# Performance work log

Hardware: AMD Instinct MI355X
Metric: run time of the kernel (lower is better)

The kernel has to match this reference:

```python
import jax, jax.numpy as jnp
import numpy as np

B, A, C, M = 8, 32768, 80, 32
VAR0, VAR1 = 0.1, 0.2          # cfg['variance']
TOPK = 50                      # pre_anchor_topk
T1 = 0.5                       # bbox_threshold
SL1_W, SL1_B = 0.75, 0.11      # smooth_l1_loss_param
ALPHA, GAMMA = 0.5, 2.0
EPS = 1e-12


def point_form(b):
    # center form (cx,cy,w,h) -> corner form (x0,y0,x1,y1)
    return jnp.concatenate([b[..., :2] - b[..., 2:] / 2,
                            b[..., :2] + b[..., 2:] / 2], axis=-1)


def decode(loc, priors):
    xy = priors[..., :2] + loc[..., :2] * VAR0 * priors[..., 2:]
    wh = priors[..., 2:] * jnp.exp(loc[..., 2:] * VAR1)
    return jnp.concatenate([xy, wh], axis=-1)  # center form


def encode(matched, priors):
    # matched: corner form, priors: center form
    g_xy = ((matched[..., :2] + matched[..., 2:]) / 2 - priors[..., :2]) / (VAR0 * priors[..., 2:])
    g_wh = jnp.log((matched[..., 2:] - matched[..., :2]) / priors[..., 2:]) / VAR1
    return jnp.concatenate([g_xy, g_wh], axis=-1)


def jaccard(a, b):
    # a: [M,4] corner, b: [A,4] corner -> IoU [M,A]
    lt = jnp.maximum(a[:, None, :2], b[None, :, :2])
    rb = jnp.minimum(a[:, None, 2:], b[None, :, 2:])
    wh = jnp.clip(rb - lt, 0.0, None)
    inter = wh[..., 0] * wh[..., 1]
    area_a = (a[:, 2] - a[:, 0]) * (a[:, 3] - a[:, 1])
    area_b = (b[:, 2] - b[:, 0]) * (b[:, 3] - b[:, 1])
    return inter / (area_a[:, None] + area_b[None, :] - inter)


def clip_st(x, lo):
    # Clip custom Function: straight-through gradient
    return x + jax.lax.stop_gradient(jnp.maximum(x, lo) - x)


def bce_log(x):
    # torch BCE clamps log at -100
    return jnp.maximum(jnp.log(jnp.clip(x, 1e-38, None)), -100.0)


def _per_image(box_reg, cls_p, tgt, lab, anchors, num_classes):
    # ---- image_box_prob (no-grad branch in original) ----
    decoded = point_form(decode(box_reg, anchors))          # [A,4]
    obi = jaccard(tgt, decoded)                             # [M,A]
    t2 = jnp.maximum(obi.max(axis=1, keepdims=True), T1 + EPS)
    obp = jnp.clip((obi - T1) / (t2 - T1), 0.0, 1.0)        # [M,A]
    # sparse per-class max over objects == segment_max on labels
    seg = jax.ops.segment_max(obp, lab, num_segments=num_classes)  # [C,A]
    image_box_prob = jax.lax.stop_gradient(jnp.maximum(seg, 0.0).T)  # [A,C]

    # ---- positive bag loss ----
    mq = jaccard(tgt, point_form(anchors))                  # [M,A]
    _, matched = jax.lax.top_k(mq, TOPK)                    # [M,K]
    cls_sel = cls_p[:, lab].T                               # [M,A] prob of own class
    matched_cls = jnp.take_along_axis(cls_sel, matched, axis=1)  # [M,K]
    pri = anchors[matched]                                  # [M,K,4]
    tgt_enc = encode(tgt[:, None, :], pri)                  # [M,K,4]
    val = tgt_enc - box_reg[matched]
    av = jnp.abs(val)
    reg_loss = SL1_W * jnp.where(av < SL1_B, 0.5 / SL1_B * val * val, av - 0.5 * SL1_B).sum(-1)
    logits = matched_cls * jnp.exp(-reg_loss)               # [M,K]
    w = 1.0 / clip_st(1.0 - logits, EPS)
    w = w / w.sum(axis=1, keepdims=True)
    bag = (w * logits).sum(axis=1)                          # [M]
    pos = -bce_log(bag)                                     # BCE(bag, 1)
    return image_box_prob, pos


def setup_inputs() -> dict:
    key = jax.random.key(0)
    k1, k2, k3, k4, k5, k6, k7 = jax.random.split(key, 7)
    box_regression = jax.random.normal(k1, (B, A, 4), jnp.float32) * 0.5
    cls_logits = jax.random.normal(k2, (B, A, C), jnp.float32) - 2.0
    a_xy = jax.random.uniform(k3, (A, 2))
    a_wh = 0.02 + 0.2 * jax.random.uniform(k4, (A, 2))
    anchors = jnp.concatenate([a_xy, a_wh], axis=-1).astype(jnp.float32)
    t_min = 0.5 * jax.random.uniform(k5, (B, M, 2))
    t_wh = 0.05 + 0.4 * jax.random.uniform(k6, (B, M, 2))
    target_boxes = jnp.concatenate([t_min, t_min + t_wh], axis=-1).astype(jnp.float32)
    labels = jax.random.randint(k7, (B, M), 0, C, dtype=jnp.int32)
    return {"box_regression": box_regression, "cls_logits": cls_logits,
            "anchors": anchors, "target_boxes": target_boxes, "labels": labels}


def reference(box_regression, cls_logits, anchors, target_boxes, labels):
    num_classes = cls_logits.shape[-1]
    cls_prob = jax.nn.sigmoid(cls_logits)                   # [B,A,C]
    box_prob, pos = jax.vmap(
        lambda br, cp, tb, lb: _per_image(br, cp, tb, lb, anchors, num_classes)
    )(box_regression, cls_prob, target_boxes, labels)       # [B,A,C], [B,M]
    positive_numels = target_boxes.shape[0] * target_boxes.shape[1]
    positive_loss = pos.sum() / max(1, positive_numels)
    p = cls_prob * (1.0 - box_prob)
    # focal_loss(p, gamma) = sum(p**gamma * BCE(p, 0)) = sum(p**gamma * -log(1-p))
    negative_loss = jnp.sum(p ** GAMMA * (-bce_log(1.0 - p))) / max(1, positive_numels * TOPK)
    return (positive_loss * ALPHA, negative_loss * (1.0 - ALPHA))
```

## Files before the change

kernel.cpp:

```cpp
#include <hip/hip_runtime.h>

#define NB 8
#define NA 32768
#define NC 80
#define NM 32
#define NK 50
#define CAP 4096
#define TB 32
#define NBLK 512
#define CORRB (NA / 256)
constexpr float VAR0 = 0.1f, VAR1 = 0.2f;
constexpr float T1f  = 0.5f;
constexpr float SL1B = 0.11f;
constexpr float SL1W = 0.75f;
constexpr float FEPS = 1e-12f;

__device__ __forceinline__ float iou_corner(float tx0, float ty0, float tx1, float ty1, float ta,
                                            float bx0, float by0, float bx1, float by1, float ba) {
  float lx = fmaxf(tx0, bx0), ly = fmaxf(ty0, by0);
  float rx = fminf(tx1, bx1), ry = fminf(ty1, by1);
  float wx = fmaxf(rx - lx, 0.f), wy = fmaxf(ry - ly, 0.f);
  float inter = wx * wy;
  return inter / (ta + ba - inter);
}

__device__ __noinline__ float anchor_iou(float4 p, float tx0, float ty0, float tx1, float ty1, float ta) {
  float hx = 0.5f * p.z, hy = 0.5f * p.w;
  float x0 = p.x - hx, y0 = p.y - hy, x1 = p.x + hx, y1 = p.y + hy;
  float ba = (x1 - x0) * (y1 - y0);
  return iou_corner(tx0, ty0, tx1, ty1, ta, x0, y0, x1, y1, ba);
}

__device__ __forceinline__ float focal_term(float s, float bp) {
  float pr = s * (1.f - bp);
  float om = fmaxf(1.f - pr, 1e-38f);
  return pr * pr * fminf(-__logf(om), 100.f);
}

__device__ __forceinline__ float focal4(float4 v) {
  float s0 = 1.f / (1.f + __expf(-v.x));
  float s1 = 1.f / (1.f + __expf(-v.y));
  float s2 = 1.f / (1.f + __expf(-v.z));
  float s3 = 1.f / (1.f + __expf(-v.w));
  return focal_term(s0, 0.f) + focal_term(s1, 0.f) + focal_term(s2, 0.f) + focal_term(s3, 0.f);
}

__global__ void __launch_bounds__(1024, 8) mega_kernel(const float4* __restrict__ br,
                                                       const float* __restrict__ cls,
                                                       const float4* __restrict__ anc,
                                                       const float4* __restrict__ tgt,
                                                       const int* __restrict__ labels,
                                                       unsigned* __restrict__ partmax,
                                                       unsigned* __restrict__ pairmask,
                                                       float* __restrict__ posp,
                                                       float* __restrict__ f0part) {
  __shared__ int hist[512];
  __shared__ unsigned long long cand[CAP];
  __shared__ int sel[NK];
  __shared__ int s_cnt, s_B1, s_filled;
  __shared__ unsigned char s_flag[1024];
  __shared__ unsigned s_max[NM];
  __shared__ float4 s_t[NM];
  __shared__ float s_ta[NM];
  __shared__ float swave[16];

  int bx = blockIdx.x;
  int tid = threadIdx.x;

  {
    const float4* cls4 = (const float4*)cls;
    constexpr int STRIDE = NBLK * 1024;
    int base = bx * 1024 + tid;
    float4 v0 = cls4[base + 0 * STRIDE];
    float4 v1 = cls4[base + 1 * STRIDE];
    float4 v2 = cls4[base + 2 * STRIDE];
    float4 v3 = cls4[base + 3 * STRIDE];
    float4 v4 = cls4[base + 4 * STRIDE];
    float accum = focal4(v0) + focal4(v1) + focal4(v2) + focal4(v3) + focal4(v4);
    float4 w0 = cls4[base + 5 * STRIDE];
    float4 w1 = cls4[base + 6 * STRIDE];
    float4 w2 = cls4[base + 7 * STRIDE];
    float4 w3 = cls4[base + 8 * STRIDE];
    float4 w4 = cls4[base + 9 * STRIDE];
    accum += focal4(w0) + focal4(w1) + focal4(w2) + focal4(w3) + focal4(w4);
    for (int off = 32; off; off >>= 1) accum += __shfl_down(accum, off);
    if ((tid & 63) == 0) swave[tid >> 6] = accum;
    __syncthreads();
    if (tid == 0) {
      float s = 0.f;
#pragma unroll
      for (int i = 0; i < 16; ++i) s += swave[i];
      f0part[bx] = s;
    }
    __syncthreads();
  }

  if (bx < NB * NM) {
    int bm = bx;
    int b = bm >> 5;
    float4 t = tgt[bm];
    float ta = (t.z - t.x) * (t.w - t.y);

    if (tid < 512) hist[tid] = 0;
    if (tid == 0) s_cnt = 0;
    __syncthreads();

    for (int a = tid; a < NA; a += 1024) {
      float iou = anchor_iou(anc[a], t.x, t.y, t.z, t.w, ta);
      if (iou > 0.f) {
        int bin = (int)(__float_as_uint(iou) >> 21);
        atomicAdd(&hist[bin], 1);
      }
    }
    __syncthreads();

    if (tid == 0) {
      int cum = 0, b1 = 0;
      for (int bin = 511; bin >= 0; --bin) {
        cum += hist[bin];
        if (cum >= NK) { b1 = bin; break; }
      }
      s_B1 = b1;
      s_filled = cum;
    }
    __syncthreads();
    int B1 = s_B1;
    bool zero_path = (s_filled < NK);

    for (int a = tid; a < NA; a += 1024) {
      float iou = anchor_iou(anc[a], t.x, t.y, t.z, t.w, ta);
      if (iou > 0.f) {
        unsigned vb = __float_as_uint(iou);
        if ((int)(vb >> 21) >= B1) {
          int slot = atomicAdd(&s_cnt, 1);
          if (slot < CAP)
            cand[slot] = ((unsigned long long)vb << 32) | (unsigned)(~a);
        }
      }
    }
    __syncthreads();
    int n = min(s_cnt, CAP);

    for (int c = tid; c < n; c += 1024) {
      unsigned long long key = cand[c];
      int rank = 0;
      for (int j = 0; j < n; ++j) rank += (cand[j] > key);
      if (rank < NK) sel[rank] = (int)(~(unsigned)(key & 0xFFFFFFFFull));
    }
    __syncthreads();

    if (zero_path) {
      if (tid == 0) s_filled = n;
      __syncthreads();
      for (int base = 0; base < NA; base += 1024) {
        int a = base + tid;
        float iou = anchor_iou(anc[a], t.x, t.y, t.z, t.w, ta);
        s_flag[tid] = (iou == 0.f);
        __syncthreads();
        if (tid == 0) {
          for (int i = 0; i < 1024 && s_filled < NK; ++i)
            if (s_flag[i]) { sel[s_filled++] = base + i; }
        }
        __syncthreads();
        if (s_filled >= NK) break;
      }
    }

    if (tid < 64) {
      int lane = tid;
      float lg = 0.f, wr = 0.f;
      if (lane < NK) {
        int a = sel[lane];
        int lb = labels[bm];
        float4 p = anc[a];
        float4 l = br[(size_t)b * NA + a];
        float logit = cls[((size_t)b * NA + a) * NC + lb];
        float mc = 1.f / (1.f + __expf(-logit));
        float gx = ((t.x + t.z) * 0.5f - p.x) / (VAR0 * p.z);
        float gy = ((t.y + t.w) * 0.5f - p.y) / (VAR0 * p.w);
        float gw = __logf((t.z - t.x) / p.z) / VAR1;
        float gh = __logf((t.w - t.y) / p.w) / VAR1;
        float v0 = gx - l.x, v1 = gy - l.y, v2 = gw - l.z, v3 = gh - l.w;
        float rl = 0.f;
        {
          float av;
          av = fabsf(v0); rl += (av < SL1B) ? (0.5f / SL1B) * v0 * v0 : (av - 0.5f * SL1B);
          av = fabsf(v1); rl += (av < SL1B) ? (0.5f / SL1B) * v1 * v1 : (av - 0.5f * SL1B);
          av = fabsf(v2); rl += (av < SL1B) ? (0.5f / SL1B) * v2 * v2 : (av - 0.5f * SL1B);
          av = fabsf(v3); rl += (av < SL1B) ? (0.5f / SL1B) * v3 * v3 : (av - 0.5f * SL1B);
        }
        rl *= SL1W;
        lg = mc * __expf(-rl);
        wr = 1.f / fmaxf(1.f - lg, FEPS);
      }
      float swl = wr * lg, swr = wr;
      for (int off = 32; off; off >>= 1) { swl += __shfl_down(swl, off); swr += __shfl_down(swr, off); }
      if (lane == 0) {
        float bag = swl / swr;
        posp[bm] = -fmaxf(logf(fmaxf(bag, 1e-38f)), -100.f);
      }
    }

  } else {
    int t2i = bx - NB * NM;
    int b = t2i >> 5;
    int chunk = t2i & 31;
    if (tid < NM) {
      float4 t = tgt[b * NM + tid];
      s_t[tid] = t;
      s_ta[tid] = (t.z - t.x) * (t.w - t.y);
      s_max[tid] = 0u;
    }
    __syncthreads();

    int a = chunk * 1024 + tid;
    float4 p = anc[a];
    float4 l = br[(size_t)b * NA + a];
    float cx = p.x + l.x * VAR0 * p.z;
    float cy = p.y + l.y * VAR0 * p.w;
    float w = p.z * __expf(l.z * VAR1);
    float h = p.w * __expf(l.w * VAR1);
    float dx0 = cx - 0.5f * w, dy0 = cy - 0.5f * h;
    float dx1 = cx + 0.5f * w, dy1 = cy + 0.5f * h;
    float da = (dx1 - dx0) * (dy1 - dy0);

    unsigned mymask = 0u;
#pragma unroll
    for (int mm = 0; mm < NM; ++mm) {
      int m = (tid + mm) & (NM - 1);
      float4 t = s_t[m];
      float iou = iou_corner(t.x, t.y, t.z, t.w, s_ta[m], dx0, dy0, dx1, dy1, da);
      if (iou > T1f) mymask |= 1u << m;
      atomicMax(&s_max[m], __float_as_uint(iou));
    }
    pairmask[(size_t)b * NA + a] = mymask;
    __syncthreads();
    if (tid < NM)
      partmax[((size_t)b * NM + tid) * TB + chunk] = s_max[tid];
  }
}

__global__ void __launch_bounds__(256) corr_kernel(const float4* __restrict__ br,
                                                   const float* __restrict__ cls,
                                                   const float4* __restrict__ anc,
                                                   const float4* __restrict__ tgt,
                                                   const int* __restrict__ labels,
                                                   const unsigned* __restrict__ partmax,
                                                   const unsigned* __restrict__ pairmask,
                                                   float* __restrict__ corrp) {
  __shared__ float4 s_t[NM];
  __shared__ float s_ta[NM], s_inv[NM];
  __shared__ unsigned s_cmask[NC];
  __shared__ unsigned s_maxm[NM];
  __shared__ unsigned s_slotmask[NM];
  __shared__ int s_slotclass[NM];
  __shared__ int s_nslots;
  int b = blockIdx.y;
  int tid = threadIdx.x;
  if (tid < NC) s_cmask[tid] = 0u;
  if (tid < NM) s_maxm[tid] = 0u;
  if (tid == 0) s_nslots = 0;
  __syncthreads();
  if (tid < NM) {
    float4 t = tgt[b * NM + tid];
    s_t[tid] = t;
    s_ta[tid] = (t.z - t.x) * (t.w - t.y);
    atomicOr(&s_cmask[labels[b * NM + tid]], 1u << tid);
  }
  {
    int m = tid >> 3, j = tid & 7;
    const unsigned* pm = &partmax[((size_t)b * NM + m) * TB];
    unsigned mx = 0u;
    for (int k = j; k < TB; k += 8) mx = max(mx, pm[k]);
    atomicMax(&s_maxm[m], mx);
  }
  __syncthreads();
  if (tid < NM) {
    float mxf = __uint_as_float(s_maxm[tid]);
    s_inv[tid] = 1.0f / (fmaxf(mxf, T1f) - T1f);
  }
  __syncthreads();
  if (tid < NC && s_cmask[tid] != 0u) {
    int slot = atomicAdd(&s_nslots, 1);
    s_slotmask[slot] = s_cmask[tid];
    s_slotclass[slot] = tid;
  }
  __syncthreads();
  int nslots = s_nslots;

  int a = blockIdx.x * 256 + tid;
  unsigned mk32 = pairmask[(size_t)b * NA + a];
  float accum = 0.f;
  if (mk32) {
    float4 p = anc[a];
    float4 l = br[(size_t)b * NA + a];
    float cx = p.x + l.x * VAR0 * p.z;
    float cy = p.y + l.y * VAR0 * p.w;
    float w = p.z * __expf(l.z * VAR1);
    float h = p.w * __expf(l.w * VAR1);
    float dx0 = cx - 0.5f * w, dy0 = cy - 0.5f * h;
    float dx1 = cx + 0.5f * w, dy1 = cy + 0.5f * h;
    float da = (dx1 - dx0) * (dy1 - dy0);
    for (int j = 0; j < nslots; ++j) {
      unsigned sm = mk32 & s_slotmask[j];
      if (!sm) continue;
      float bp = 0.f;
      while (sm) {
        int m = __ffs(sm) - 1;
        sm &= sm - 1;
        float4 t = s_t[m];
        float iou = iou_corner(t.x, t.y, t.z, t.w, s_ta[m], dx0, dy0, dx1, dy1, da);
        float o = (iou - T1f) * s_inv[m];
        bp = fmaxf(bp, fminf(fmaxf(o, 0.f), 1.f));
      }
      if (bp > 0.f) {
        float logit = cls[((size_t)b * NA + a) * NC + s_slotclass[j]];
        float s = 1.f / (1.f + __expf(-logit));
        accum += focal_term(s, bp) - focal_term(s, 0.f);
      }
    }
  }
  for (int off = 32; off; off >>= 1) accum += __shfl_down(accum, off);
  __shared__ float swv[4];
  if ((tid & 63) == 0) swv[tid >> 6] = accum;
  __syncthreads();
  if (tid == 0)
    corrp[(size_t)b * CORRB + blockIdx.x] = swv[0] + swv[1] + swv[2] + swv[3];
}

__global__ void __launch_bounds__(256) fin_kernel(const float* __restrict__ posp,
                                                  const float* __restrict__ f0part,
                                                  const float* __restrict__ corrp,
                                                  float* __restrict__ out) {
  int tid = threadIdx.x;
  double sp = 0.0, sn = 0.0;
  for (int i = tid; i < NB * NM; i += 256) sp += (double)posp[i];
  for (int i = tid; i < NBLK; i += 256) sn += (double)f0part[i];
  for (int i = tid; i < NB * CORRB; i += 256) sn += (double)corrp[i];
  for (int off = 32; off; off >>= 1) { sp += __shfl_down(sp, off); sn += __shfl_down(sn, off); }
  __shared__ double swp[4], swn[4];
  if ((tid & 63) == 0) { swp[tid >> 6] = sp; swn[tid >> 6] = sn; }
  __syncthreads();
  if (tid == 0) {
    double pos = swp[0] + swp[1] + swp[2] + swp[3];
    double neg = swn[0] + swn[1] + swn[2] + swn[3];
    out[0] = (float)(pos / 256.0 * 0.5);
    out[1] = (float)(neg / 12800.0 * 0.5);
  }
}

extern "C" void kernel_launch(void* const* d_in, const int* in_sizes, int n_in,
                              void* d_out, int out_size, void* d_ws, size_t ws_size,
                              hipStream_t stream) {
  const float4* br  = (const float4*)d_in[0];
  const float*  cls = (const float*)d_in[1];
  const float4* anc = (const float4*)d_in[2];
  const float4* tgt = (const float4*)d_in[3];
  const int*    lab = (const int*)d_in[4];
  float* out = (float*)d_out;
  float*    posp     = (float*)d_ws;
  float*    f0part   = (float*)((char*)d_ws + 4096);
  float*    corrp    = (float*)((char*)d_ws + 8192);
  unsigned* partmax  = (unsigned*)((char*)d_ws + 16384);
  unsigned* pairmask = (unsigned*)((char*)d_ws + 65536);

  mega_kernel<<<dim3(NBLK), 1024, 0, stream>>>(
      br, cls, anc, tgt, lab, partmax, pairmask, posp, f0part);
  corr_kernel<<<dim3(CORRB, NB), 256, 0, stream>>>(br, cls, anc, tgt, lab, partmax, pairmask, corrp);
  fin_kernel<<<1, 256, 0, stream>>>(posp, f0part, corrp, out);
}
```

Before: 58.57 us.

## Split per-object top-k selection across two anchor halves with merge kernel

Each (image, object) top-k search is now split across two blocks, each scanning half the anchors, and the grid doubles so the focal-loss sweep needs half as many loads per thread. A bitmask of positive-IoU anchors from the histogram pass lets the second pass recompute IoU only for those anchors and lets the zero-fill path skip IoU entirely. A new small kernel merges the two per-half top-50 candidate lists, fills any shortfall with zero-IoU anchors, and computes the positive bag loss. This adds a kernel launch and global round-trips for the candidates, and halves the shared candidate capacity.

```diff
diff --git a/kernel.cpp b/kernel.cpp
--- a/kernel.cpp
+++ b/kernel.cpp
@@ -5,9 +5,10 @@
 #define NC 80
 #define NM 32
 #define NK 50
-#define CAP 4096
+#define CAP 2048
 #define TB 32
-#define NBLK 512
+#define HALF_A (NA / 2)
+#define NBLK 1024
 #define CORRB (NA / 256)
 constexpr float VAR0 = 0.1f, VAR1 = 0.2f;
 constexpr float T1f  = 0.5f;
@@ -49,15 +50,16 @@
                                                        const float* __restrict__ cls,
                                                        const float4* __restrict__ anc,
                                                        const float4* __restrict__ tgt,
-                                                       const int* __restrict__ labels,
                                                        unsigned* __restrict__ partmax,
                                                        unsigned* __restrict__ pairmask,
-                                                       float* __restrict__ posp,
+                                                       unsigned long long* __restrict__ cand50,
+                                                       unsigned* __restrict__ poscnt,
+                                                       unsigned* __restrict__ zlist,
+                                                       unsigned* __restrict__ zcnt,
                                                        float* __restrict__ f0part) {
   __shared__ int hist[512];
   __shared__ unsigned long long cand[CAP];
-  __shared__ int sel[NK];
-  __shared__ int s_cnt, s_B1, s_filled;
+  __shared__ int s_cnt, s_B1, s_filled, s_zc;
   __shared__ unsigned char s_flag[1024];
   __shared__ unsigned s_max[NM];
   __shared__ float4 s_t[NM];
@@ -77,12 +79,6 @@
     float4 v3 = cls4[base + 3 * STRIDE];
     float4 v4 = cls4[base + 4 * STRIDE];
     float accum = focal4(v0) + focal4(v1) + focal4(v2) + focal4(v3) + focal4(v4);
-    float4 w0 = cls4[base + 5 * STRIDE];
-    float4 w1 = cls4[base + 6 * STRIDE];
-    float4 w2 = cls4[base + 7 * STRIDE];
-    float4 w3 = cls4[base + 8 * STRIDE];
-    float4 w4 = cls4[base + 9 * STRIDE];
-    accum += focal4(w0) + focal4(w1) + focal4(w2) + focal4(w3) + focal4(w4);
     for (int off = 32; off; off >>= 1) accum += __shfl_down(accum, off);
     if ((tid & 63) == 0) swave[tid >> 6] = accum;
     __syncthreads();
@@ -95,9 +91,11 @@
     __syncthreads();
   }
 
-  if (bx < NB * NM) {
-    int bm = bx;
-    int b = bm >> 5;
+  if (bx < 2 * NB * NM) {
+    int bm = bx >> 1;
+    int half = bx & 1;
+    int abase = half * HALF_A;
+    int b = bm >> 5; (void)b;
     float4 t = tgt[bm];
     float ta = (t.z - t.x) * (t.w - t.y);
 
@@ -105,11 +103,13 @@
     if (tid == 0) s_cnt = 0;
     __syncthreads();
 
-    for (int a = tid; a < NA; a += 1024) {
+    unsigned mask = 0u;
+    for (int k = 0; k < 16; ++k) {
+      int a = abase + tid + (k << 10);
       float iou = anchor_iou(anc[a], t.x, t.y, t.z, t.w, ta);
       if (iou > 0.f) {
-        int bin = (int)(__float_as_uint(iou) >> 21);
-        atomicAdd(&hist[bin], 1);
+        mask |= 1u << k;
+        atomicAdd(&hist[(int)(__float_as_uint(iou) >> 21)], 1);
       }
     }
     __syncthreads();
@@ -125,11 +125,16 @@
     }
     __syncthreads();
     int B1 = s_B1;
-    bool zero_path = (s_filled < NK);
-
-    for (int a = tid; a < NA; a += 1024) {
-      float iou = anchor_iou(anc[a], t.x, t.y, t.z, t.w, ta);
-      if (iou > 0.f) {
+    int local_pos = s_filled;
+    if (tid == 0) poscnt[bm * 2 + half] = (unsigned)min(local_pos, NK);
+
+    {
+      unsigned msk = mask;
+      while (msk) {
+        int k = __ffs(msk) - 1;
+        msk &= msk - 1;
+        int a = abase + tid + (k << 10);
+        float iou = anchor_iou(anc[a], t.x, t.y, t.z, t.w, ta);
         unsigned vb = __float_as_uint(iou);
         if ((int)(vb >> 21) >= B1) {
           int slot = atomicAdd(&s_cnt, 1);
@@ -145,64 +150,29 @@
       unsigned long long key = cand[c];
       int rank = 0;
       for (int j = 0; j < n; ++j) rank += (cand[j] > key);
-      if (rank < NK) sel[rank] = (int)(~(unsigned)(key & 0xFFFFFFFFull));
-    }
-    __syncthreads();
-
-    if (zero_path) {
-      if (tid == 0) s_filled = n;
+      if (rank < NK) cand50[(size_t)(bm * 2 + half) * NK + rank] = key;
+    }
+    int nw = min(n, NK);
+    if (tid >= nw && tid < NK)
+      cand50[(size_t)(bm * 2 + half) * NK + tid] = 0ull;
+
+    if (local_pos < NK) {
+      if (tid == 0) s_zc = 0;
       __syncthreads();
-      for (int base = 0; base < NA; base += 1024) {
-        int a = base + tid;
-        float iou = anchor_iou(anc[a], t.x, t.y, t.z, t.w, ta);
-        s_flag[tid] = (iou == 0.f);
+      for (int k = 0; k < 16; ++k) {
+        s_flag[tid] = ((mask >> k) & 1u) == 0u;
         __syncthreads();
         if (tid == 0) {
-          for (int i = 0; i < 1024 && s_filled < NK; ++i)
-            if (s_flag[i]) { sel[s_filled++] = base + i; }
+          for (int i = 0; i < 1024 && s_zc < NK; ++i)
+            if (s_flag[i]) zlist[(size_t)(bm * 2 + half) * NK + s_zc++] = abase + (k << 10) + i;
         }
         __syncthreads();
-        if (s_filled >= NK) break;
-      }
-    }
-
-    if (tid < 64) {
-      int lane = tid;
-      float lg = 0.f, wr = 0.f;
-      if (lane < NK) {
-        int a = sel[lane];
-        int lb = labels[bm];
-        float4 p = anc[a];
-        float4 l = br[(size_t)b * NA + a];
-        float logit = cls[((size_t)b * NA + a) * NC + lb];
-        float mc = 1.f / (1.f + __expf(-logit));
-        float gx = ((t.x + t.z) * 0.5f - p.x) / (VAR0 * p.z);
-        float gy = ((t.y + t.w) * 0.5f - p.y) / (VAR0 * p.w);
-        float gw = __logf((t.z - t.x) / p.z) / VAR1;
-        float gh = __logf((t.w - t.y) / p.w) / VAR1;
-        float v0 = gx - l.x, v1 = gy - l.y, v2 = gw - l.z, v3 = gh - l.w;
-        float rl = 0.f;
-        {
-          float av;
-          av = fabsf(v0); rl += (av < SL1B) ? (0.5f / SL1B) * v0 * v0 : (av - 0.5f * SL1B);
-          av = fabsf(v1); rl += (av < SL1B) ? (0.5f / SL1B) * v1 * v1 : (av - 0.5f * SL1B);
-          av = fabsf(v2); rl += (av < SL1B) ? (0.5f / SL1B) * v2 * v2 : (av - 0.5f * SL1B);
-          av = fabsf(v3); rl += (av < SL1B) ? (0.5f / SL1B) * v3 * v3 : (av - 0.5f * SL1B);
-        }
-        rl *= SL1W;
-        lg = mc * __expf(-rl);
-        wr = 1.f / fmaxf(1.f - lg, FEPS);
-      }
-      float swl = wr * lg, swr = wr;
-      for (int off = 32; off; off >>= 1) { swl += __shfl_down(swl, off); swr += __shfl_down(swr, off); }
-      if (lane == 0) {
-        float bag = swl / swr;
-        posp[bm] = -fmaxf(logf(fmaxf(bag, 1e-38f)), -100.f);
-      }
-    }
-
-  } else {
-    int t2i = bx - NB * NM;
+      }
+      if (tid == 0) zcnt[bm * 2 + half] = (unsigned)s_zc;
+    }
+
+  } else if (bx < 2 * NB * NM + TB * NB) {
+    int t2i = bx - 2 * NB * NM;
     int b = t2i >> 5;
     int chunk = t2i & 31;
     if (tid < NM) {
@@ -237,6 +207,89 @@
     __syncthreads();
     if (tid < NM)
       partmax[((size_t)b * NM + tid) * TB + chunk] = s_max[tid];
+  }
+}
+
+__global__ void __launch_bounds__(128) posfin_kernel(const float4* __restrict__ br,
+                                                     const float* __restrict__ cls,
+                                                     const float4* __restrict__ anc,
+                                                     const float4* __restrict__ tgt,
+                                                     const int* __restrict__ labels,
+                                                     const unsigned long long* __restrict__ cand50,
+                                                     const unsigned* __restrict__ poscnt,
+                                                     const unsigned* __restrict__ zlist,
+                                                     const unsigned* __restrict__ zcnt,
+                                                     float* __restrict__ posp) {
+  __shared__ unsigned long long kbuf[2 * NK];
+  __shared__ int sel[NK];
+  __shared__ int s_total;
+  int bm = blockIdx.x;
+  int b = bm >> 5;
+  int tid = threadIdx.x;
+  float4 t = tgt[bm];
+
+  if (tid < NK) {
+    kbuf[tid]      = cand50[(size_t)(bm * 2 + 0) * NK + tid];
+    kbuf[NK + tid] = cand50[(size_t)(bm * 2 + 1) * NK + tid];
+  }
+  if (tid == 0)
+    s_total = (int)(poscnt[bm * 2] + poscnt[bm * 2 + 1]);
+  __syncthreads();
+
+  if (tid < 2 * NK) {
+    unsigned long long key = kbuf[tid];
+    if (key != 0ull) {
+      int rank = 0;
+      for (int j = 0; j < 2 * NK; ++j) rank += (kbuf[j] > key);
+      if (rank < NK) sel[rank] = (int)(~(unsigned)(key & 0xFFFFFFFFull));
+    }
+  }
+  __syncthreads();
+
+  int total = s_total;
+  if (total < NK) {
+    if (tid == 0) {
+      int idx = total;
+      unsigned zc0 = zcnt[bm * 2], zc1 = zcnt[bm * 2 + 1];
+      for (unsigned j = 0; j < zc0 && idx < NK; ++j) sel[idx++] = (int)zlist[(size_t)(bm * 2) * NK + j];
+      for (unsigned j = 0; j < zc1 && idx < NK; ++j) sel[idx++] = (int)zlist[(size_t)(bm * 2 + 1) * NK + j];
+    }
+    __syncthreads();
+  }
+
+  if (tid < 64) {
+    int lane = tid;
+    float lg = 0.f, wr = 0.f;
+    if (lane < NK) {
+      int a = sel[lane];
+      int lb = labels[bm];
+      float4 p = anc[a];
+      float4 l = br[(size_t)b * NA + a];
+      float logit = cls[((size_t)b * NA + a) * NC + lb];
+      float mc = 1.f / (1.f + __expf(-logit));
+      float gx = ((t.x + t.z) * 0.5f - p.x) / (VAR0 * p.z);
+      float gy = ((t.y + t.w) * 0.5f - p.y) / (VAR0 * p.w);
+      float gw = __logf((t.z - t.x) / p.z) / VAR1;
+      float gh = __logf((t.w - t.y) / p.w) / VAR1;
+      float v0 = gx - l.x, v1 = gy - l.y, v2 = gw - l.z, v3 = gh - l.w;
+      float rl = 0.f;
+      {
+        float av;
+        av = fabsf(v0); rl += (av < SL1B) ? (0.5f / SL1B) * v0 * v0 : (av - 0.5f * SL1B);
+        av = fabsf(v1); rl += (av < SL1B) ? (0.5f / SL1B) * v1 * v1 : (av - 0.5f * SL1B);
+        av = fabsf(v2); rl += (av < SL1B) ? (0.5f / SL1B) * v2 * v2 : (av - 0.5f * SL1B);
+        av = fabsf(v3); rl += (av < SL1B) ? (0.5f / SL1B) * v3 * v3 : (av - 0.5f * SL1B);
+      }
+      rl *= SL1W;
+      lg = mc * __expf(-rl);
+      wr = 1.f / fmaxf(1.f - lg, FEPS);
+    }
+    float swl = wr * lg, swr = wr;
+    for (int off = 32; off; off >>= 1) { swl += __shfl_down(swl, off); swr += __shfl_down(swr, off); }
+    if (lane == 0) {
+      float bag = swl / swr;
+      posp[bm] = -fmaxf(logf(fmaxf(bag, 1e-38f)), -100.f);
+    }
   }
 }
 
@@ -358,14 +411,20 @@
   const float4* tgt = (const float4*)d_in[3];
   const int*    lab = (const int*)d_in[4];
   float* out = (float*)d_out;
-  float*    posp     = (float*)d_ws;
-  float*    f0part   = (float*)((char*)d_ws + 4096);
-  float*    corrp    = (float*)((char*)d_ws + 8192);
-  unsigned* partmax  = (unsigned*)((char*)d_ws + 16384);
-  unsigned* pairmask = (unsigned*)((char*)d_ws + 65536);
+  float*              posp     = (float*)d_ws;
+  float*              f0part   = (float*)((char*)d_ws + 4096);
+  float*              corrp    = (float*)((char*)d_ws + 8192);
+  unsigned*           poscnt   = (unsigned*)((char*)d_ws + 12288);
+  unsigned*           partmax  = (unsigned*)((char*)d_ws + 16384);
+  unsigned long long* cand50   = (unsigned long long*)((char*)d_ws + 49152);
+  unsigned*           zlist    = (unsigned*)((char*)d_ws + 253952);
+  unsigned*           zcnt     = (unsigned*)((char*)d_ws + 356352);
+  unsigned*           pairmask = (unsigned*)((char*)d_ws + 360448);
 
   mega_kernel<<<dim3(NBLK), 1024, 0, stream>>>(
-      br, cls, anc, tgt, lab, partmax, pairmask, posp, f0part);
+      br, cls, anc, tgt, partmax, pairmask, cand50, poscnt, zlist, zcnt, f0part);
+  posfin_kernel<<<dim3(NB * NM), 128, 0, stream>>>(
+      br, cls, anc, tgt, lab, cand50, poscnt, zlist, zcnt, posp);
   corr_kernel<<<dim3(CORRB, NB), 256, 0, stream>>>(br, cls, anc, tgt, lab, partmax, pairmask, corrp);
   fin_kernel<<<1, 256, 0, stream>>>(posp, f0part, corrp, out);
 }
```

After: 61.59 us. 5.2% more time.
